# Kernel tuning notes

Hardware: AMD Instinct MI355X
Metric: run time of the kernel (lower is better)

The kernel has to match this reference:

```python
import jax, jax.numpy as jnp
import numpy as np

SCALE = 8.0  # sqrt(d_head=64), per init_kwargs
B, H, S, D = 2, 16, 2048, 64


def setup_inputs() -> dict:
    key = jax.random.key(0)
    kq, kk, kv = jax.random.split(key, 3)
    q = jax.random.normal(kq, (B, H, S, D), dtype=jnp.float32)
    k = jax.random.normal(kk, (B, H, S, D), dtype=jnp.float32)
    v = jax.random.normal(kv, (B, H, S, D), dtype=jnp.float32)
    # causal mask: True where attention is NOT allowed (strictly upper triangle)
    causal = jnp.triu(jnp.ones((S, S), dtype=bool), k=1)
    mask = jnp.broadcast_to(causal, (B, H, S, S))
    return {"q": q, "k": k, "v": v, "mask": mask}


def reference(q, k, v, mask):
    # score = (q @ k^T) / scale, masked_fill(mask, -inf), softmax, @ v
    score = jnp.einsum('bhqd,bhkd->bhqk', q, k) / SCALE
    score = jnp.where(mask, -jnp.inf, score)
    attn = jax.nn.softmax(score, axis=-1)
    output = jnp.einsum('bhqk,bhkd->bhqd', attn, v)
    return (attn, output)
```

## Files before the change

### kernel.cpp

```cpp
#include <hip/hip_runtime.h>
#include <hip/hip_bf16.h>

#define S_LEN 2048
#define D_HEAD 64
#define SD (S_LEN * D_HEAD)
#define TILE_B 8192
#define NTILES 32

typedef __attribute__((ext_vector_type(8))) short short8;
typedef __attribute__((ext_vector_type(4))) float f32x4;

__device__ __forceinline__ unsigned short f2b(float f) {
  unsigned int u = __float_as_uint(f);
  u += 0x7fffu + ((u >> 16) & 1u);
  return (unsigned short)(u >> 16);
}

__device__ __forceinline__ float b2f(unsigned short s) {
  return __uint_as_float(((unsigned int)s) << 16);
}

__device__ __forceinline__ void nt_store4(float* p, f32x4 v) {
  __builtin_nontemporal_store(v, (f32x4*)p);
}

__device__ __forceinline__ void gl_lds16(const void* g, void* l) {
  __builtin_amdgcn_global_load_lds(
      (const __attribute__((address_space(1))) unsigned int*)g,
      (__attribute__((address_space(3))) unsigned int*)l, 16, 0, 0);
}

__device__ __forceinline__ void stage8k(const char* gsrc, char* ldst, int w, int lane) {
  gl_lds16(gsrc + ((w * 64 + lane) << 4),        ldst + ((w * 64) << 4));
  gl_lds16(gsrc + ((256 + w * 64 + lane) << 4),  ldst + ((256 + w * 64) << 4));
}

__global__ __launch_bounds__(256) void convert_kv_kernel(
    const float* __restrict__ K, const float* __restrict__ V,
    char* __restrict__ Kpre, char* __restrict__ Vpre) {
  const int bid = blockIdx.x;
  const int tid = threadIdx.x;
  if (bid < 1024) {
    const int bh = bid >> 5, tile = bid & 31;
    const float* Kb = K + (size_t)bh * SD + tile * 64 * 64;
    char* out = Kpre + (size_t)bid * TILE_B;
    #pragma unroll
    for (int j = 0; j < 2; ++j) {
      int c = tid + j * 256;
      int sl = c >> 3;
      int d0 = ((c & 7) ^ (sl & 7)) << 3;
      const float* src = Kb + sl * 64 + d0;
      float4 a = *(const float4*)src;
      float4 b = *(const float4*)(src + 4);
      short8 o;
      o[0]=(short)f2b(a.x); o[1]=(short)f2b(a.y); o[2]=(short)f2b(a.z); o[3]=(short)f2b(a.w);
      o[4]=(short)f2b(b.x); o[5]=(short)f2b(b.y); o[6]=(short)f2b(b.z); o[7]=(short)f2b(b.w);
      *(short8*)(out + c * 16) = o;
    }
  } else {
    __shared__ float Vl[64][65];
    const int vb = bid - 1024;
    const int bh = vb >> 5, tile = vb & 31;
    const float* Vb = V + (size_t)bh * SD + tile * 64 * 64;
    #pragma unroll
    for (int j = 0; j < 4; ++j) {
      int row = (tid >> 4) + j * 16;
      int c4 = (tid & 15) << 2;
      float4 v = *(const float4*)(Vb + row * 64 + c4);
      Vl[row][c4+0] = v.x; Vl[row][c4+1] = v.y; Vl[row][c4+2] = v.z; Vl[row][c4+3] = v.w;
    }
    __syncthreads();
    char* out = Vpre + (size_t)vb * TILE_B;
    #pragma unroll
    for (int j = 0; j < 2; ++j) {
      int c = tid + j * 256;
      int d = c >> 3;
      int s0 = ((c & 7) ^ ((d >> 2) & 7)) << 3;
      short8 o;
      #pragma unroll
      for (int i = 0; i < 8; ++i) o[i] = (short)f2b(Vl[s0 + i][d]);
      *(short8*)(out + c * 16) = o;
    }
  }
}

__global__ __launch_bounds__(256, 4) void sdpa_pre_kernel(
    const float* __restrict__ Qg, const char* __restrict__ Kpre,
    const char* __restrict__ Vpre, float* __restrict__ attn,
    float* __restrict__ outp) {
  const int j  = blockIdx.x >> 8;
  const int rr = blockIdx.x & 255;
  const int xcd = rr & 7;
  const int cu  = rr >> 3;
  const int bh  = xcd + ((cu & 3) << 3);
  const int u   = cu >> 2;
  const int qt  = (j == 0) ? u : (j == 1) ? (15 - u) : (j == 2) ? (16 + u) : (31 - u);

  const int tid = threadIdx.x, wave = tid >> 6, lane = tid & 63;
  const int g = lane >> 4, m = lane & 15;
  const int swzK = (m & 7) << 4;

  __shared__ __align__(16) unsigned short Ring[4][4096];
  __shared__ __align__(16) unsigned short Pl[4][1024];
  char* const RB = (char*)Ring;
  char* const PB = (char*)(&Pl[wave][0]);

  const size_t bhSD = (size_t)bh * SD;
  const size_t bhSS = (size_t)bh << 22;
  const char* KpreBH = Kpre + (size_t)bh * NTILES * TILE_B;
  const char* VpreBH = Vpre + (size_t)bh * NTILES * TILE_B;

  int vro[4], vsz[4];
  #pragma unroll
  for (int dc = 0; dc < 4; ++dc) {
    int d = dc * 16 + m;
    vro[dc] = d << 7;
    vsz[dc] = ((d >> 2) & 7) << 4;
  }
  const float SCL = 0.18033688011112042f;

  const int q0 = qt << 6;
  const int nIt = qt + 1;
  const int qwrow = q0 + wave * 16;
  const int qbase = qwrow + g * 4;

  short8 aq0, aq1;
  {
    const float* qp = Qg + bhSD + (size_t)(qwrow + m) * D_HEAD + g * 8;
    float4 x0 = *(const float4*)(qp);
    float4 x1 = *(const float4*)(qp + 4);
    float4 y0 = *(const float4*)(qp + 32);
    float4 y1 = *(const float4*)(qp + 36);
    aq0[0]=(short)f2b(x0.x*SCL); aq0[1]=(short)f2b(x0.y*SCL);
    aq0[2]=(short)f2b(x0.z*SCL); aq0[3]=(short)f2b(x0.w*SCL);
    aq0[4]=(short)f2b(x1.x*SCL); aq0[5]=(short)f2b(x1.y*SCL);
    aq0[6]=(short)f2b(x1.z*SCL); aq0[7]=(short)f2b(x1.w*SCL);
    aq1[0]=(short)f2b(y0.x*SCL); aq1[1]=(short)f2b(y0.y*SCL);
    aq1[2]=(short)f2b(y0.z*SCL); aq1[3]=(short)f2b(y0.w*SCL);
    aq1[4]=(short)f2b(y1.x*SCL); aq1[5]=(short)f2b(y1.y*SCL);
    aq1[6]=(short)f2b(y1.z*SCL); aq1[7]=(short)f2b(y1.w*SCL);
  }

  float rs0 = 0.f, rs1 = 0.f, rs2 = 0.f, rs3 = 0.f;
  {
    const int npre = nIt < 3 ? nIt : 3;
    for (int t0 = 0; t0 < npre; ++t0)
      stage8k(KpreBH + (size_t)t0 * TILE_B, RB + t0 * TILE_B, wave, lane);
  }
  for (int it = 0; it < nIt; ++it) {
    if (it + 2 < nIt)      { asm volatile("s_waitcnt vmcnt(4)" ::: "memory"); }
    else if (it + 1 < nIt) { asm volatile("s_waitcnt vmcnt(2)" ::: "memory"); }
    else                   { asm volatile("s_waitcnt vmcnt(0)" ::: "memory"); }
    __builtin_amdgcn_s_barrier();
    __builtin_amdgcn_sched_barrier(0);
    if (it + 3 < nIt)
      stage8k(KpreBH + (size_t)(it + 3) * TILE_B, RB + ((it + 3) & 3) * TILE_B, wave, lane);
    asm volatile("" ::: "memory");
    const char* KB = RB + (it & 3) * TILE_B;
    const int kc = it << 6;
    if (kc + 64 <= qwrow) {
      #pragma unroll
      for (int t = 0; t < 4; ++t) {
        f32x4 acc = {0.f, 0.f, 0.f, 0.f};
        const int rb = (t * 16 + m) << 7;
        short8 b0 = *(const short8*)(KB + ((rb + g * 16) ^ swzK));
        short8 b1 = *(const short8*)(KB + ((rb + 64 + g * 16) ^ swzK));
        acc = __builtin_amdgcn_mfma_f32_16x16x32_bf16(aq0, b0, acc, 0, 0, 0);
        acc = __builtin_amdgcn_mfma_f32_16x16x32_bf16(aq1, b1, acc, 0, 0, 0);
        rs0 += exp2f(acc[0]);
        rs1 += exp2f(acc[1]);
        rs2 += exp2f(acc[2]);
        rs3 += exp2f(acc[3]);
      }
    } else {
      #pragma unroll
      for (int t = 0; t < 4; ++t) {
        f32x4 acc = {0.f, 0.f, 0.f, 0.f};
        const int rb = (t * 16 + m) << 7;
        short8 b0 = *(const short8*)(KB + ((rb + g * 16) ^ swzK));
        short8 b1 = *(const short8*)(KB + ((rb + 64 + g * 16) ^ swzK));
        acc = __builtin_amdgcn_mfma_f32_16x16x32_bf16(aq0, b0, acc, 0, 0, 0);
        acc = __builtin_amdgcn_mfma_f32_16x16x32_bf16(aq1, b1, acc, 0, 0, 0);
        const int kcol = kc + t * 16 + m;
        rs0 += (kcol <= qbase + 0) ? exp2f(acc[0]) : 0.f;
        rs1 += (kcol <= qbase + 1) ? exp2f(acc[1]) : 0.f;
        rs2 += (kcol <= qbase + 2) ? exp2f(acc[2]) : 0.f;
        rs3 += (kcol <= qbase + 3) ? exp2f(acc[3]) : 0.f;
      }
    }
  }
  #pragma unroll
  for (int sft = 1; sft < 16; sft <<= 1) {
    rs0 += __shfl_xor(rs0, sft, 64);
    rs1 += __shfl_xor(rs1, sft, 64);
    rs2 += __shfl_xor(rs2, sft, 64);
    rs3 += __shfl_xor(rs3, sft, 64);
  }
  const float ri0 = 1.f / rs0, ri1 = 1.f / rs1, ri2 = 1.f / rs2, ri3 = 1.f / rs3;

  f32x4 o0 = {0.f,0.f,0.f,0.f}, o1 = {0.f,0.f,0.f,0.f};
  f32x4 o2 = {0.f,0.f,0.f,0.f}, o3 = {0.f,0.f,0.f,0.f};
  __builtin_amdgcn_s_barrier();
  stage8k(KpreBH, RB + 0 * TILE_B, wave, lane);
  stage8k(VpreBH, RB + 2 * TILE_B, wave, lane);
  int cur = 0;
  const int r4 = lane >> 4;
  const int cf = (lane & 15) << 2;
  for (int it = 0; it < nIt; ++it) {
    if (it == 0) { asm volatile("s_waitcnt vmcnt(0)" ::: "memory"); }
    else         { asm volatile("s_waitcnt vmcnt(16)" ::: "memory"); }
    __builtin_amdgcn_s_barrier();
    __builtin_amdgcn_sched_barrier(0);
    if (it + 1 < nIt) {
      stage8k(KpreBH + (size_t)(it + 1) * TILE_B, RB + (cur ^ 1) * TILE_B, wave, lane);
      stage8k(VpreBH + (size_t)(it + 1) * TILE_B, RB + (2 + (cur ^ 1)) * TILE_B, wave, lane);
    }
    asm volatile("" ::: "memory");
    const char* KB = RB + cur * TILE_B;
    const char* VB = RB + (2 + cur) * TILE_B;
    const int kc = it << 6;
    if (kc + 64 <= qwrow) {
      #pragma unroll
      for (int t = 0; t < 4; ++t) {
        f32x4 acc = {0.f, 0.f, 0.f, 0.f};
        const int rb = (t * 16 + m) << 7;
        short8 b0 = *(const short8*)(KB + ((rb + g * 16) ^ swzK));
        short8 b1 = *(const short8*)(KB + ((rb + 64 + g * 16) ^ swzK));
        acc = __builtin_amdgcn_mfma_f32_16x16x32_bf16(aq0, b0, acc, 0, 0, 0);
        acc = __builtin_amdgcn_mfma_f32_16x16x32_bf16(aq1, b1, acc, 0, 0, 0);
        float p0 = exp2f(acc[0]) * ri0;
        float p1 = exp2f(acc[1]) * ri1;
        float p2 = exp2f(acc[2]) * ri2;
        float p3 = exp2f(acc[3]) * ri3;
        const int r0 = g * 4, c2 = (t * 16 + m) << 1;
        *(unsigned short*)(PB + ((((r0+0)<<7) + c2) ^ (((r0+0)&7)<<4))) = f2b(p0);
        *(unsigned short*)(PB + ((((r0+1)<<7) + c2) ^ (((r0+1)&7)<<4))) = f2b(p1);
        *(unsigned short*)(PB + ((((r0+2)<<7) + c2) ^ (((r0+2)&7)<<4))) = f2b(p2);
        *(unsigned short*)(PB + ((((r0+3)<<7) + c2) ^ (((r0+3)&7)<<4))) = f2b(p3);
      }
    } else {
      #pragma unroll
      for (int t = 0; t < 4; ++t) {
        f32x4 acc = {0.f, 0.f, 0.f, 0.f};
        const int rb = (t * 16 + m) << 7;
        short8 b0 = *(const short8*)(KB + ((rb + g * 16) ^ swzK));
        short8 b1 = *(const short8*)(KB + ((rb + 64 + g * 16) ^ swzK));
        acc = __builtin_amdgcn_mfma_f32_16x16x32_bf16(aq0, b0, acc, 0, 0, 0);
        acc = __builtin_amdgcn_mfma_f32_16x16x32_bf16(aq1, b1, acc, 0, 0, 0);
        const int kcol = kc + t * 16 + m;
        float p0 = (kcol <= qbase + 0) ? exp2f(acc[0]) * ri0 : 0.f;
        float p1 = (kcol <= qbase + 1) ? exp2f(acc[1]) * ri1 : 0.f;
        float p2 = (kcol <= qbase + 2) ? exp2f(acc[2]) * ri2 : 0.f;
        float p3 = (kcol <= qbase + 3) ? exp2f(acc[3]) * ri3 : 0.f;
        const int r0 = g * 4, c2 = (t * 16 + m) << 1;
        *(unsigned short*)(PB + ((((r0+0)<<7) + c2) ^ (((r0+0)&7)<<4))) = f2b(p0);
        *(unsigned short*)(PB + ((((r0+1)<<7) + c2) ^ (((r0+1)&7)<<4))) = f2b(p1);
        *(unsigned short*)(PB + ((((r0+2)<<7) + c2) ^ (((r0+2)&7)<<4))) = f2b(p2);
        *(unsigned short*)(PB + ((((r0+3)<<7) + c2) ^ (((r0+3)&7)<<4))) = f2b(p3);
      }
    }
    {
      float* abase2 = attn + bhSS + (size_t)qwrow * S_LEN + kc;
      #pragma unroll
      for (int jj = 0; jj < 4; ++jj) {
        const int row = 4 * jj + r4;
        const int off = (((row << 7) + (cf << 1))) ^ ((row & 7) << 4);
        ushort4 pr = *(const ushort4*)(PB + off);
        f32x4 fa;
        fa[0] = b2f(pr.x); fa[1] = b2f(pr.y); fa[2] = b2f(pr.z); fa[3] = b2f(pr.w);
        nt_store4(abase2 + (size_t)row * S_LEN + cf, fa);
      }
    }
    short8 pa0 = *(const short8*)(PB + (((m << 7) + g * 16) ^ swzK));
    short8 pa1 = *(const short8*)(PB + (((m << 7) + 64 + g * 16) ^ swzK));
    #pragma unroll
    for (int dc = 0; dc < 4; ++dc) {
      short8 bv0 = *(const short8*)(VB + ((vro[dc] + g * 16) ^ vsz[dc]));
      short8 bv1 = *(const short8*)(VB + ((vro[dc] + 64 + g * 16) ^ vsz[dc]));
      f32x4& od = (dc == 0) ? o0 : (dc == 1) ? o1 : (dc == 2) ? o2 : o3;
      od = __builtin_amdgcn_mfma_f32_16x16x32_bf16(pa0, bv0, od, 0, 0, 0);
      od = __builtin_amdgcn_mfma_f32_16x16x32_bf16(pa1, bv1, od, 0, 0, 0);
    }
    cur ^= 1;
  }

  #pragma unroll
  for (int reg = 0; reg < 4; ++reg) {
    float* op = outp + bhSD + (size_t)(qbase + reg) * D_HEAD + m;
    __builtin_nontemporal_store(o0[reg], op +  0);
    __builtin_nontemporal_store(o1[reg], op + 16);
    __builtin_nontemporal_store(o2[reg], op + 32);
    __builtin_nontemporal_store(o3[reg], op + 48);
  }

  const int col0 = nIt << 6;
  const int nvec = (S_LEN - col0) >> 2;
  if (nvec > 0) {
    const f32x4 z = {0.f, 0.f, 0.f, 0.f};
    for (int r = 0; r < 64; ++r) {
      float* rp = attn + bhSS + (size_t)(q0 + r) * S_LEN + col0;
      for (int i = tid; i < nvec; i += 256) nt_store4(rp + i * 4, z);
    }
  }
}

__global__ __launch_bounds__(256) void sdpa_fb_kernel(
    const float* __restrict__ Qg, const float* __restrict__ Kg,
    const float* __restrict__ Vg, float* __restrict__ attn,
    float* __restrict__ outp) {
  const int bh = blockIdx.x >> 4;
  const int pi = blockIdx.x & 15;
  const int tid  = threadIdx.x;
  const int wave = tid >> 6;
  const int lane = tid & 63;
  const int g = lane >> 4;
  const int m = lane & 15;
  const int swzK = (m & 7) << 4;
  __shared__ __align__(16) unsigned short Kl[2][64 * 64];
  __shared__ __align__(16) unsigned short Vt[2][64 * 64];
  __shared__ __align__(16) unsigned short Pl[4][16 * 64];
  char* const PB = (char*)(&Pl[wave][0]);
  const size_t bhSD = (size_t)bh * (S_LEN * D_HEAD);
  const size_t bhSS = (size_t)bh * ((size_t)S_LEN * S_LEN);
  int ss[4], dd[4], koff[4];
  #pragma unroll
  for (int j = 0; j < 4; ++j) {
    int f = tid + j * 256;
    ss[j] = f >> 4;
    dd[j] = (f & 15) << 2;
    koff[j] = (((ss[j] << 6) + dd[j]) << 1) ^ ((ss[j] & 7) << 4);
  }
  int vro[4], vsz[4];
  #pragma unroll
  for (int dc = 0; dc < 4; ++dc) {
    int d = dc * 16 + m;
    vro[dc] = d << 7;
    vsz[dc] = ((d >> 2) & 7) << 4;
  }
  const float SCL = 0.18033688011112042f;
  for (int sidx = 0; sidx < 2; ++sidx) {
    const int qt = sidx ? (31 - pi) : pi;
    const int q0 = qt << 6;
    const int kmax = q0 + 64;
    const int nIter = kmax >> 6;
    const int qwrow = q0 + wave * 16;
    const int qbase = qwrow + g * 4;
    short8 aq0, aq1;
    {
      const float* qp = Qg + bhSD + (size_t)(qwrow + m) * D_HEAD + g * 8;
      float4 x0 = *(const float4*)(qp);
      float4 x1 = *(const float4*)(qp + 4);
      float4 y0 = *(const float4*)(qp + 32);
      float4 y1 = *(const float4*)(qp + 36);
      aq0[0]=(short)f2b(x0.x*SCL); aq0[1]=(short)f2b(x0.y*SCL);
      aq0[2]=(short)f2b(x0.z*SCL); aq0[3]=(short)f2b(x0.w*SCL);
      aq0[4]=(short)f2b(x1.x*SCL); aq0[5]=(short)f2b(x1.y*SCL);
      aq0[6]=(short)f2b(x1.z*SCL); aq0[7]=(short)f2b(x1.w*SCL);
      aq1[0]=(short)f2b(y0.x*SCL); aq1[1]=(short)f2b(y0.y*SCL);
      aq1[2]=(short)f2b(y0.z*SCL); aq1[3]=(short)f2b(y0.w*SCL);
      aq1[4]=(short)f2b(y1.x*SCL); aq1[5]=(short)f2b(y1.y*SCL);
      aq1[6]=(short)f2b(y1.z*SCL); aq1[7]=(short)f2b(y1.w*SCL);
    }
    float rs0 = 0.f, rs1 = 0.f, rs2 = 0.f, rs3 = 0.f;
    {
      float4 kr[4];
      #pragma unroll
      for (int j = 0; j < 4; ++j)
        kr[j] = *(const float4*)(Kg + bhSD + (size_t)ss[j] * D_HEAD + dd[j]);
      #pragma unroll
      for (int j = 0; j < 4; ++j) {
        ushort4 kb;
        kb.x = f2b(kr[j].x); kb.y = f2b(kr[j].y);
        kb.z = f2b(kr[j].z); kb.w = f2b(kr[j].w);
        *(ushort4*)((char*)Kl[0] + koff[j]) = kb;
      }
    }
    __syncthreads();
    int cur = 0;
    for (int it = 0; it < nIter; ++it) {
      const int kc = it << 6;
      const bool pf = (it + 1 < nIter);
      float4 kr[4];
      if (pf) {
        #pragma unroll
        for (int j = 0; j < 4; ++j)
          kr[j] = *(const float4*)(Kg + bhSD + (size_t)(kc + 64 + ss[j]) * D_HEAD + dd[j]);
      }
      const char* KB = (const char*)Kl[cur];
      #pragma unroll
      for (int t = 0; t < 4; ++t) {
        f32x4 acc = {0.f, 0.f, 0.f, 0.f};
        const int rb = (t * 16 + m) << 7;
        short8 b0 = *(const short8*)(KB + ((rb + g * 16) ^ swzK));
        short8 b1 = *(const short8*)(KB + ((rb + 64 + g * 16) ^ swzK));
        acc = __builtin_amdgcn_mfma_f32_16x16x32_bf16(aq0, b0, acc, 0, 0, 0);
        acc = __builtin_amdgcn_mfma_f32_16x16x32_bf16(aq1, b1, acc, 0, 0, 0);
        const int kcol = kc + t * 16 + m;
        rs0 += (kcol <= qbase + 0) ? exp2f(acc[0]) : 0.f;
        rs1 += (kcol <= qbase + 1) ? exp2f(acc[1]) : 0.f;
        rs2 += (kcol <= qbase + 2) ? exp2f(acc[2]) : 0.f;
        rs3 += (kcol <= qbase + 3) ? exp2f(acc[3]) : 0.f;
      }
      if (pf) {
        #pragma unroll
        for (int j = 0; j < 4; ++j) {
          ushort4 kb;
          kb.x = f2b(kr[j].x); kb.y = f2b(kr[j].y);
          kb.z = f2b(kr[j].z); kb.w = f2b(kr[j].w);
          *(ushort4*)((char*)Kl[cur ^ 1] + koff[j]) = kb;
        }
      }
      __syncthreads();
      cur ^= 1;
    }
    #pragma unroll
    for (int sft = 1; sft < 16; sft <<= 1) {
      rs0 += __shfl_xor(rs0, sft, 64);
      rs1 += __shfl_xor(rs1, sft, 64);
      rs2 += __shfl_xor(rs2, sft, 64);
      rs3 += __shfl_xor(rs3, sft, 64);
    }
    const float ri0 = 1.f / rs0, ri1 = 1.f / rs1, ri2 = 1.f / rs2, ri3 = 1.f / rs3;
    f32x4 o0 = {0.f,0.f,0.f,0.f}, o1 = {0.f,0.f,0.f,0.f};
    f32x4 o2 = {0.f,0.f,0.f,0.f}, o3 = {0.f,0.f,0.f,0.f};
    {
      float4 kr[4], vr[4];
      #pragma unroll
      for (int j = 0; j < 4; ++j) {
        kr[j] = *(const float4*)(Kg + bhSD + (size_t)ss[j] * D_HEAD + dd[j]);
        vr[j] = *(const float4*)(Vg + bhSD + (size_t)ss[j] * D_HEAD + dd[j]);
      }
      #pragma unroll
      for (int j = 0; j < 4; ++j) {
        ushort4 kb;
        kb.x = f2b(kr[j].x); kb.y = f2b(kr[j].y);
        kb.z = f2b(kr[j].z); kb.w = f2b(kr[j].w);
        *(ushort4*)((char*)Kl[0] + koff[j]) = kb;
        const int d0 = dd[j], s2 = ss[j] << 1;
        char* VB1 = (char*)Vt[0];
        *(unsigned short*)(VB1 + ((((d0+0)<<7) + s2) ^ ((((d0+0)>>2)&7)<<4))) = f2b(vr[j].x);
        *(unsigned short*)(VB1 + ((((d0+1)<<7) + s2) ^ ((((d0+1)>>2)&7)<<4))) = f2b(vr[j].y);
        *(unsigned short*)(VB1 + ((((d0+2)<<7) + s2) ^ ((((d0+2)>>2)&7)<<4))) = f2b(vr[j].z);
        *(unsigned short*)(VB1 + ((((d0+3)<<7) + s2) ^ ((((d0+3)>>2)&7)<<4))) = f2b(vr[j].w);
      }
    }
    __syncthreads();
    cur = 0;
    for (int it = 0; it < nIter; ++it) {
      const int kc = it << 6;
      const bool pf = (it + 1 < nIter);
      float4 kr[4], vr[4];
      if (pf) {
        #pragma unroll
        for (int j = 0; j < 4; ++j) {
          kr[j] = *(const float4*)(Kg + bhSD + (size_t)(kc + 64 + ss[j]) * D_HEAD + dd[j]);
          vr[j] = *(const float4*)(Vg + bhSD + (size_t)(kc + 64 + ss[j]) * D_HEAD + dd[j]);
        }
      }
      const char* KB = (const char*)Kl[cur];
      const char* VB = (const char*)Vt[cur];
      float* arow = attn + bhSS + (size_t)qbase * S_LEN + kc;
      #pragma unroll
      for (int t = 0; t < 4; ++t) {
        f32x4 acc = {0.f, 0.f, 0.f, 0.f};
        const int rb = (t * 16 + m) << 7;
        short8 b0 = *(const short8*)(KB + ((rb + g * 16) ^ swzK));
        short8 b1 = *(const short8*)(KB + ((rb + 64 + g * 16) ^ swzK));
        acc = __builtin_amdgcn_mfma_f32_16x16x32_bf16(aq0, b0, acc, 0, 0, 0);
        acc = __builtin_amdgcn_mfma_f32_16x16x32_bf16(aq1, b1, acc, 0, 0, 0);
        const int kcol = kc + t * 16 + m;
        const int tc = t * 16 + m;
        float p0 = (kcol <= qbase + 0) ? exp2f(acc[0]) * ri0 : 0.f;
        float p1 = (kcol <= qbase + 1) ? exp2f(acc[1]) * ri1 : 0.f;
        float p2 = (kcol <= qbase + 2) ? exp2f(acc[2]) * ri2 : 0.f;
        float p3 = (kcol <= qbase + 3) ? exp2f(acc[3]) * ri3 : 0.f;
        arow[0 * S_LEN + tc] = p0;
        arow[1 * S_LEN + tc] = p1;
        arow[2 * S_LEN + tc] = p2;
        arow[3 * S_LEN + tc] = p3;
        const int r0 = g * 4, c2 = tc << 1;
        *(unsigned short*)(PB + ((((r0+0)<<7) + c2) ^ (((r0+0)&7)<<4))) = f2b(p0);
        *(unsigned short*)(PB + ((((r0+1)<<7) + c2) ^ (((r0+1)&7)<<4))) = f2b(p1);
        *(unsigned short*)(PB + ((((r0+2)<<7) + c2) ^ (((r0+2)&7)<<4))) = f2b(p2);
        *(unsigned short*)(PB + ((((r0+3)<<7) + c2) ^ (((r0+3)&7)<<4))) = f2b(p3);
      }
      short8 pa0 = *(const short8*)(PB + (((m << 7) + g * 16) ^ swzK));
      short8 pa1 = *(const short8*)(PB + (((m << 7) + 64 + g * 16) ^ swzK));
      #pragma unroll
      for (int dc = 0; dc < 4; ++dc) {
        short8 bv0 = *(const short8*)(VB + ((vro[dc] + g * 16) ^ vsz[dc]));
        short8 bv1 = *(const short8*)(VB + ((vro[dc] + 64 + g * 16) ^ vsz[dc]));
        f32x4& od = (dc == 0) ? o0 : (dc == 1) ? o1 : (dc == 2) ? o2 : o3;
        od = __builtin_amdgcn_mfma_f32_16x16x32_bf16(pa0, bv0, od, 0, 0, 0);
        od = __builtin_amdgcn_mfma_f32_16x16x32_bf16(pa1, bv1, od, 0, 0, 0);
      }
      if (pf) {
        #pragma unroll
        for (int j = 0; j < 4; ++j) {
          ushort4 kb;
          kb.x = f2b(kr[j].x); kb.y = f2b(kr[j].y);
          kb.z = f2b(kr[j].z); kb.w = f2b(kr[j].w);
          *(ushort4*)((char*)Kl[cur ^ 1] + koff[j]) = kb;
          const int d0 = dd[j], s2 = ss[j] << 1;
          char* VB1 = (char*)Vt[cur ^ 1];
          *(unsigned short*)(VB1 + ((((d0+0)<<7) + s2) ^ ((((d0+0)>>2)&7)<<4))) = f2b(vr[j].x);
          *(unsigned short*)(VB1 + ((((d0+1)<<7) + s2) ^ ((((d0+1)>>2)&7)<<4))) = f2b(vr[j].y);
          *(unsigned short*)(VB1 + ((((d0+2)<<7) + s2) ^ ((((d0+2)>>2)&7)<<4))) = f2b(vr[j].z);
          *(unsigned short*)(VB1 + ((((d0+3)<<7) + s2) ^ ((((d0+3)>>2)&7)<<4))) = f2b(vr[j].w);
        }
      }
      __syncthreads();
      cur ^= 1;
    }
    #pragma unroll
    for (int reg = 0; reg < 4; ++reg) {
      float* op = outp + bhSD + (size_t)(qbase + reg) * D_HEAD + m;
      op[ 0] = o0[reg];
      op[16] = o1[reg];
      op[32] = o2[reg];
      op[48] = o3[reg];
    }
    const int ncols = S_LEN - kmax;
    if (ncols > 0) {
      const float4 z = {0.f, 0.f, 0.f, 0.f};
      const int nvec = ncols >> 2;
      for (int r = 0; r < 64; ++r) {
        float4* rp = (float4*)(attn + bhSS + (size_t)(q0 + r) * S_LEN + kmax);
        for (int i = tid; i < nvec; i += 256) rp[i] = z;
      }
    }
  }
}

extern "C" void kernel_launch(void* const* d_in, const int* in_sizes, int n_in,
                              void* d_out, int out_size, void* d_ws, size_t ws_size,
                              hipStream_t stream) {
  (void)in_sizes; (void)n_in; (void)out_size;
  const float* q = (const float*)d_in[0];
  const float* k = (const float*)d_in[1];
  const float* v = (const float*)d_in[2];
  float* attn = (float*)d_out;
  float* outp = attn + (size_t)2 * 16 * 2048 * 2048;
  const size_t pre_bytes = (size_t)32 * NTILES * TILE_B;
  if (ws_size >= 2 * pre_bytes) {
    char* Kpre = (char*)d_ws;
    char* Vpre = Kpre + pre_bytes;
    convert_kv_kernel<<<2048, 256, 0, stream>>>(k, v, Kpre, Vpre);
    sdpa_pre_kernel<<<1024, 256, 0, stream>>>(q, Kpre, Vpre, attn, outp);
  } else {
    sdpa_fb_kernel<<<512, 256, 0, stream>>>(q, k, v, attn, outp);
  }
}
```

Baseline: 152.4 us.

## Dedicate wave 0 to K/V staging and move zero-fill of masked attn to the start

All global-to-LDS staging of K and V tiles is now issued by wave 0 alone, with 8 loads per tile instead of 2 per wave, and its vmcnt waits are adjusted to match. Waves 1-3 write the zero region of the attention matrix at the start of the kernel rather than at the end. The aim is to overlap the large zero-store traffic with the main loops and keep the other waves' memory counters free of staging loads. In exchange, wave 0 becomes the sole issuer of staging loads, and the early zero stores from waves 1-3 compete with it for memory bandwidth.

After: 153.0 us. About the same (+0.4%).

```diff
diff --git a/kernel.cpp b/kernel.cpp
--- a/kernel.cpp
+++ b/kernel.cpp
@@ -30,9 +30,10 @@
       (__attribute__((address_space(3))) unsigned int*)l, 16, 0, 0);
 }
 
-__device__ __forceinline__ void stage8k(const char* gsrc, char* ldst, int w, int lane) {
-  gl_lds16(gsrc + ((w * 64 + lane) << 4),        ldst + ((w * 64) << 4));
-  gl_lds16(gsrc + ((256 + w * 64 + lane) << 4),  ldst + ((256 + w * 64) << 4));
+__device__ __forceinline__ void stage8k_w0(const char* gsrc, char* ldst, int lane) {
+  #pragma unroll
+  for (int k = 0; k < 8; ++k)
+    gl_lds16(gsrc + ((k * 64 + lane) << 4), ldst + ((k * 64) << 4));
 }
 
 __global__ __launch_bounds__(256) void convert_kv_kernel(
@@ -141,20 +142,33 @@
     aq1[6]=(short)f2b(y1.z*SCL); aq1[7]=(short)f2b(y1.w*SCL);
   }
 
+  const int col0 = nIt << 6;
+  const int nvec = (S_LEN - col0) >> 2;
+  if (wave > 0 && nvec > 0) {
+    const f32x4 z = {0.f, 0.f, 0.f, 0.f};
+    const int lt = (wave - 1) * 64 + lane;
+    for (int r = 0; r < 64; ++r) {
+      float* rp = attn + bhSS + (size_t)(q0 + r) * S_LEN + col0;
+      for (int i = lt; i < nvec; i += 192) nt_store4(rp + i * 4, z);
+    }
+  }
+
   float rs0 = 0.f, rs1 = 0.f, rs2 = 0.f, rs3 = 0.f;
-  {
+  if (wave == 0) {
     const int npre = nIt < 3 ? nIt : 3;
     for (int t0 = 0; t0 < npre; ++t0)
-      stage8k(KpreBH + (size_t)t0 * TILE_B, RB + t0 * TILE_B, wave, lane);
+      stage8k_w0(KpreBH + (size_t)t0 * TILE_B, RB + t0 * TILE_B, lane);
   }
   for (int it = 0; it < nIt; ++it) {
-    if (it + 2 < nIt)      { asm volatile("s_waitcnt vmcnt(4)" ::: "memory"); }
-    else if (it + 1 < nIt) { asm volatile("s_waitcnt vmcnt(2)" ::: "memory"); }
-    else                   { asm volatile("s_waitcnt vmcnt(0)" ::: "memory"); }
+    if (wave == 0) {
+      if (it + 2 < nIt)      { asm volatile("s_waitcnt vmcnt(16)" ::: "memory"); }
+      else if (it + 1 < nIt) { asm volatile("s_waitcnt vmcnt(8)" ::: "memory"); }
+      else                   { asm volatile("s_waitcnt vmcnt(0)" ::: "memory"); }
+    }
     __builtin_amdgcn_s_barrier();
     __builtin_amdgcn_sched_barrier(0);
-    if (it + 3 < nIt)
-      stage8k(KpreBH + (size_t)(it + 3) * TILE_B, RB + ((it + 3) & 3) * TILE_B, wave, lane);
+    if (wave == 0 && it + 3 < nIt)
+      stage8k_w0(KpreBH + (size_t)(it + 3) * TILE_B, RB + ((it + 3) & 3) * TILE_B, lane);
     asm volatile("" ::: "memory");
     const char* KB = RB + (it & 3) * TILE_B;
     const int kc = it << 6;
@@ -201,19 +215,23 @@
   f32x4 o0 = {0.f,0.f,0.f,0.f}, o1 = {0.f,0.f,0.f,0.f};
   f32x4 o2 = {0.f,0.f,0.f,0.f}, o3 = {0.f,0.f,0.f,0.f};
   __builtin_amdgcn_s_barrier();
-  stage8k(KpreBH, RB + 0 * TILE_B, wave, lane);
-  stage8k(VpreBH, RB + 2 * TILE_B, wave, lane);
+  if (wave == 0) {
+    stage8k_w0(KpreBH, RB + 0 * TILE_B, lane);
+    stage8k_w0(VpreBH, RB + 2 * TILE_B, lane);
+  }
   int cur = 0;
   const int r4 = lane >> 4;
   const int cf = (lane & 15) << 2;
   for (int it = 0; it < nIt; ++it) {
-    if (it == 0) { asm volatile("s_waitcnt vmcnt(0)" ::: "memory"); }
-    else         { asm volatile("s_waitcnt vmcnt(16)" ::: "memory"); }
+    if (wave == 0) {
+      if (it == 0) { asm volatile("s_waitcnt vmcnt(0)" ::: "memory"); }
+      else         { asm volatile("s_waitcnt vmcnt(16)" ::: "memory"); }
+    }
     __builtin_amdgcn_s_barrier();
     __builtin_amdgcn_sched_barrier(0);
-    if (it + 1 < nIt) {
-      stage8k(KpreBH + (size_t)(it + 1) * TILE_B, RB + (cur ^ 1) * TILE_B, wave, lane);
-      stage8k(VpreBH + (size_t)(it + 1) * TILE_B, RB + (2 + (cur ^ 1)) * TILE_B, wave, lane);
+    if (wave == 0 && it + 1 < nIt) {
+      stage8k_w0(KpreBH + (size_t)(it + 1) * TILE_B, RB + (cur ^ 1) * TILE_B, lane);
+      stage8k_w0(VpreBH + (size_t)(it + 1) * TILE_B, RB + (2 + (cur ^ 1)) * TILE_B, lane);
     }
     asm volatile("" ::: "memory");
     const char* KB = RB + cur * TILE_B;
@@ -291,16 +309,6 @@
     __builtin_nontemporal_store(o1[reg], op + 16);
     __builtin_nontemporal_store(o2[reg], op + 32);
     __builtin_nontemporal_store(o3[reg], op + 48);
-  }
-
-  const int col0 = nIt << 6;
-  const int nvec = (S_LEN - col0) >> 2;
-  if (nvec > 0) {
-    const f32x4 z = {0.f, 0.f, 0.f, 0.f};
-    for (int r = 0; r < 64; ++r) {
-      float* rp = attn + bhSS + (size_t)(q0 + r) * S_LEN + col0;
-      for (int i = tid; i < nvec; i += 256) nt_store4(rp + i * 4, z);
-    }
   }
 }
 
```
